# Optimization experiments

Hardware: AMD Instinct MI355X
Metric: run time of the kernel (lower is better)

Reference implementation:

```python
import jax, jax.numpy as jnp
import numpy as np
import math

H = 16          # num_attention_heads
DH = 64         # attention_head_size
HID = 1024      # hidden_size


def _rotate_half(x):
    # stack([-x[...,1::2], x[...,::2]], -1).reshape_as(x)
    return jnp.stack([-x[..., 1::2], x[..., ::2]], axis=-1).reshape(x.shape)


def _apply_rope(sinusoidal_pos, q, k):
    sin, cos = jnp.split(sinusoidal_pos, 2, axis=-1)            # [1,1,S,DH/2] each
    sin_pos = jnp.stack([sin, sin], axis=-1).reshape(sinusoidal_pos.shape)
    cos_pos = jnp.stack([cos, cos], axis=-1).reshape(sinusoidal_pos.shape)
    q = q * cos_pos + _rotate_half(q) * sin_pos
    k = k * cos_pos + _rotate_half(k) * sin_pos
    return q, k


def _split_heads(x):
    B, S, _ = x.shape
    return x.reshape(B, S, H, DH).transpose(0, 2, 1, 3)         # [B,H,S,DH]


def setup_inputs() -> dict:
    key = jax.random.key(0)
    ks = jax.random.split(key, 5)
    B, S = 4, 2048
    x = jax.random.normal(ks[0], (B, S, HID), dtype=jnp.float32)
    attention_mask = jnp.zeros((B, 1, 1, S), dtype=jnp.float32)
    sinusoidal_pos = jax.random.normal(ks[1], (1, 1, S, DH), dtype=jnp.float32)
    scale = 1.0 / math.sqrt(HID)
    Wq = jax.random.normal(ks[2], (HID, HID), dtype=jnp.float32) * scale
    Wk = jax.random.normal(ks[3], (HID, HID), dtype=jnp.float32) * scale
    Wv = jax.random.normal(ks[4], (HID, HID), dtype=jnp.float32) * scale
    bq = jnp.zeros((HID,), dtype=jnp.float32)
    bk = jnp.zeros((HID,), dtype=jnp.float32)
    bv = jnp.zeros((HID,), dtype=jnp.float32)
    return {"x": x, "attention_mask": attention_mask, "sinusoidal_pos": sinusoidal_pos,
            "Wq": Wq, "bq": bq, "Wk": Wk, "bk": bk, "Wv": Wv, "bv": bv}


def reference(x, attention_mask, sinusoidal_pos, Wq, bq, Wk, bk, Wv, bv):
    # QKV projections (torch Linear: x @ W.T + b)
    q = _split_heads(x @ Wq.T + bq)                             # [B,H,S,DH]
    k = _split_heads(x @ Wk.T + bk)
    v = _split_heads(x @ Wv.T + bv)
    q, k = _apply_rope(sinusoidal_pos, q, k)
    scores = jnp.einsum('bhsd,bhtd->bhst', q, k) / math.sqrt(DH) + attention_mask
    probs = jax.nn.softmax(scores, axis=-1)                     # dropout p=0.0 -> identity
    ctx = jnp.einsum('bhst,bhtd->bhsd', probs, v)               # [B,H,S,DH]
    B, _, S, _ = ctx.shape
    return ctx.transpose(0, 2, 1, 3).reshape(B, S, HID)
```

## Files before the change

### kernel.cpp

```cpp
#include <hip/hip_runtime.h>
#include <stdint.h>

#define BATCH 4
#define SEQ   2048
#define NHEAD 16
#define DHEAD 64
#define HID   1024

typedef __bf16 bf16x8 __attribute__((ext_vector_type(8)));
typedef __bf16 bf16x4 __attribute__((ext_vector_type(4)));
typedef float  f32x4  __attribute__((ext_vector_type(4)));
typedef short  s16x4  __attribute__((ext_vector_type(4)));

__device__ __forceinline__ bf16x8 load8f(const float* p) {
  const f32x4 a = ((const f32x4*)p)[0];
  const f32x4 b = ((const f32x4*)p)[1];
  bf16x8 r;
#pragma unroll
  for (int i = 0; i < 4; ++i) r[i] = (__bf16)a[i];
#pragma unroll
  for (int i = 0; i < 4; ++i) r[4 + i] = (__bf16)b[i];
  return r;
}

__device__ __forceinline__ s16x4 as_s16x4(bf16x4 v) {
  s16x4 r; __builtin_memcpy(&r, &v, 8); return r;
}

__device__ __forceinline__ void gload_lds16(const __bf16* g, __bf16* l) {
  __builtin_amdgcn_global_load_lds(
      (const __attribute__((address_space(1))) uint32_t*)g,
      (__attribute__((address_space(3))) uint32_t*)l,
      16, 0, 0);
}

#define XUNITS 1048576
#define WUNITS 131072

__global__ __launch_bounds__(256) void cvt_fused_kernel(
    const float* __restrict__ x,
    const float* __restrict__ Wq, const float* __restrict__ Wk,
    const float* __restrict__ Wv,
    __bf16* __restrict__ xb, __bf16* __restrict__ Wb) {
  const int i = blockIdx.x * 256 + threadIdx.x;
  const float* s;
  __bf16* d;
  if (i < XUNITS) {
    s = x + (size_t)i * 8;
    d = xb + (size_t)i * 8;
  } else {
    const int j = i - XUNITS;
    const int w = j >> 17;
    const int o = j & (WUNITS - 1);
    s = (w == 0 ? Wq : w == 1 ? Wk : Wv) + (size_t)o * 8;
    d = Wb + ((size_t)w << 20) + (size_t)o * 8;
  }
  *(bf16x8*)d = load8f(s);
}

#define ASTRIDE 40
#define BK 32

__global__ __launch_bounds__(512) void qkv_fused_kernel(
    const __bf16* __restrict__ xb, const __bf16* __restrict__ Wb,
    const float* __restrict__ bq, const float* __restrict__ bk,
    const float* __restrict__ bv, const float* __restrict__ sp,
    float* __restrict__ qout, __bf16* __restrict__ Kws, __bf16* __restrict__ Vws)
{
  const int d    = blockIdx.x + (blockIdx.y << 3);
  const int t    = (d & 7) * 64 + (d >> 3);
  const int n0   = (t & 7) * 128;
  const int m0   = (t >> 3) * 128;

  const int tid  = threadIdx.x;
  const int lane = tid & 63;
  const int quad = lane >> 4;
  const int l16  = lane & 15;
  const int wave = tid >> 6;
  const int wr   = wave >> 1, wc = wave & 1;

  __shared__ __align__(16) __bf16 As[2][128 * BK];
  __shared__ __align__(16) __bf16 Bs[3][2][128 * BK];

  const int srow = wave * 16 + (lane >> 2);
  const int scol = (lane & 3) * 8;
  const __bf16* aglb  = xb + (size_t)(m0 + srow) * HID + scol;
  const __bf16* bglb0 = Wb + (size_t)(n0 + srow) * HID + scol;
  const __bf16* bglb1 = bglb0 + (size_t)HID * HID;
  const __bf16* bglb2 = bglb0 + (size_t)2 * HID * HID;
  const int woff = wave * 512;

  f32x4 aQ[2][4], aK[2][4], aV[2][4];
  const f32x4 z = {0.f, 0.f, 0.f, 0.f};
#pragma unroll
  for (int i = 0; i < 2; ++i)
#pragma unroll
    for (int j = 0; j < 4; ++j) { aQ[i][j] = z; aK[i][j] = z; aV[i][j] = z; }

  gload_lds16(aglb,  &As[0][woff]);
  gload_lds16(bglb0, &Bs[0][0][woff]);
  gload_lds16(bglb1, &Bs[1][0][woff]);
  gload_lds16(bglb2, &Bs[2][0][woff]);
  __syncthreads();

#pragma unroll 1
  for (int k0 = 0; k0 < HID; k0 += 2 * BK) {
    {
      gload_lds16(aglb  + (k0 + BK), &As[1][woff]);
      gload_lds16(bglb0 + (k0 + BK), &Bs[0][1][woff]);
      gload_lds16(bglb1 + (k0 + BK), &Bs[1][1][woff]);
      gload_lds16(bglb2 + (k0 + BK), &Bs[2][1][woff]);

      bf16x8 af[2];
#pragma unroll
      for (int mt = 0; mt < 2; ++mt)
        af[mt] = *(const bf16x8*)(&As[0][(wr * 32 + mt * 16 + l16) * BK + quad * 8]);
      {
        bf16x8 bfr[4];
#pragma unroll
        for (int nt = 0; nt < 4; ++nt)
          bfr[nt] = *(const bf16x8*)(&Bs[0][0][(wc * 64 + nt * 16 + l16) * BK + quad * 8]);
#pragma unroll
        for (int mt = 0; mt < 2; ++mt)
#pragma unroll
          for (int nt = 0; nt < 4; ++nt)
            aQ[mt][nt] = __builtin_amdgcn_mfma_f32_16x16x32_bf16(af[mt], bfr[nt], aQ[mt][nt], 0, 0, 0);
      }
      {
        bf16x8 bfr[4];
#pragma unroll
        for (int nt = 0; nt < 4; ++nt)
          bfr[nt] = *(const bf16x8*)(&Bs[1][0][(wc * 64 + nt * 16 + l16) * BK + quad * 8]);
#pragma unroll
        for (int mt = 0; mt < 2; ++mt)
#pragma unroll
          for (int nt = 0; nt < 4; ++nt)
            aK[mt][nt] = __builtin_amdgcn_mfma_f32_16x16x32_bf16(af[mt], bfr[nt], aK[mt][nt], 0, 0, 0);
      }
      {
        bf16x8 bfr[4];
#pragma unroll
        for (int nt = 0; nt < 4; ++nt)
          bfr[nt] = *(const bf16x8*)(&Bs[2][0][(wc * 64 + nt * 16 + l16) * BK + quad * 8]);
#pragma unroll
        for (int mt = 0; mt < 2; ++mt)
#pragma unroll
          for (int nt = 0; nt < 4; ++nt)
            aV[mt][nt] = __builtin_amdgcn_mfma_f32_16x16x32_bf16(bfr[nt], af[mt], aV[mt][nt], 0, 0, 0);
      }
      __syncthreads();
    }
    {
      if (k0 + 2 * BK < HID) {
        gload_lds16(aglb  + (k0 + 2 * BK), &As[0][woff]);
        gload_lds16(bglb0 + (k0 + 2 * BK), &Bs[0][0][woff]);
        gload_lds16(bglb1 + (k0 + 2 * BK), &Bs[1][0][woff]);
        gload_lds16(bglb2 + (k0 + 2 * BK), &Bs[2][0][woff]);
      }

      bf16x8 af[2];
#pragma unroll
      for (int mt = 0; mt < 2; ++mt)
        af[mt] = *(const bf16x8*)(&As[1][(wr * 32 + mt * 16 + l16) * BK + quad * 8]);
      {
        bf16x8 bfr[4];
#pragma unroll
        for (int nt = 0; nt < 4; ++nt)
          bfr[nt] = *(const bf16x8*)(&Bs[0][1][(wc * 64 + nt * 16 + l16) * BK + quad * 8]);
#pragma unroll
        for (int mt = 0; mt < 2; ++mt)
#pragma unroll
          for (int nt = 0; nt < 4; ++nt)
            aQ[mt][nt] = __builtin_amdgcn_mfma_f32_16x16x32_bf16(af[mt], bfr[nt], aQ[mt][nt], 0, 0, 0);
      }
      {
        bf16x8 bfr[4];
#pragma unroll
        for (int nt = 0; nt < 4; ++nt)
          bfr[nt] = *(const bf16x8*)(&Bs[1][1][(wc * 64 + nt * 16 + l16) * BK + quad * 8]);
#pragma unroll
        for (int mt = 0; mt < 2; ++mt)
#pragma unroll
          for (int nt = 0; nt < 4; ++nt)
            aK[mt][nt] = __builtin_amdgcn_mfma_f32_16x16x32_bf16(af[mt], bfr[nt], aK[mt][nt], 0, 0, 0);
      }
      {
        bf16x8 bfr[4];
#pragma unroll
        for (int nt = 0; nt < 4; ++nt)
          bfr[nt] = *(const bf16x8*)(&Bs[2][1][(wc * 64 + nt * 16 + l16) * BK + quad * 8]);
#pragma unroll
        for (int mt = 0; mt < 2; ++mt)
#pragma unroll
          for (int nt = 0; nt < 4; ++nt)
            aV[mt][nt] = __builtin_amdgcn_mfma_f32_16x16x32_bf16(bfr[nt], af[mt], aV[mt][nt], 0, 0, 0);
      }
      __syncthreads();
    }
  }

#pragma unroll
  for (int mt = 0; mt < 2; ++mt) {
#pragma unroll
    for (int nt = 0; nt < 4; ++nt) {
      const int n = n0 + wc * 64 + nt * 16 + l16;
      const int h = n >> 6, dd = n & 63;
      const float bval = bq[n];
#pragma unroll
      for (int v = 0; v < 4; ++v) {
        const int m = m0 + wr * 32 + mt * 16 + quad * 4 + v;
        const int b = m >> 11, s = m & (SEQ - 1);
        float val = aQ[mt][nt][v] + bval;
        float p  = __shfl_xor(val, 1);
        float sn = sp[s * 64 + (dd >> 1)];
        float cs = sp[s * 64 + 32 + (dd >> 1)];
        val = val * cs + ((dd & 1) ? p : -p) * sn;
        qout[((size_t)b * SEQ + s) * HID + n] = val;
      }
    }
  }
#pragma unroll
  for (int mt = 0; mt < 2; ++mt) {
#pragma unroll
    for (int nt = 0; nt < 4; ++nt) {
      const int n = n0 + wc * 64 + nt * 16 + l16;
      const int h = n >> 6, dd = n & 63;
      const float bval = bk[n];
#pragma unroll
      for (int v = 0; v < 4; ++v) {
        const int m = m0 + wr * 32 + mt * 16 + quad * 4 + v;
        const int b = m >> 11, s = m & (SEQ - 1);
        float val = aK[mt][nt][v] + bval;
        float p  = __shfl_xor(val, 1);
        float sn = sp[s * 64 + (dd >> 1)];
        float cs = sp[s * 64 + 32 + (dd >> 1)];
        val = val * cs + ((dd & 1) ? p : -p) * sn;
        Kws[(((size_t)b * NHEAD + h) * SEQ + s) * DHEAD + dd] = (__bf16)val;
      }
    }
  }
#pragma unroll
  for (int mt = 0; mt < 2; ++mt) {
#pragma unroll
    for (int nt = 0; nt < 4; ++nt) {
      const int m = m0 + wr * 32 + mt * 16 + l16;
      const int b = m >> 11, s = m & (SEQ - 1);
#pragma unroll
      for (int v = 0; v < 4; ++v) {
        const int n = n0 + wc * 64 + nt * 16 + quad * 4 + v;
        const int h = n >> 6, dd = n & 63;
        float val = aV[mt][nt][v] + bv[n];
        Vws[(((size_t)b * NHEAD + h) * DHEAD + dd) * SEQ + s] = (__bf16)val;
      }
    }
  }
}

__global__ __launch_bounds__(512) void qkv_f32_kernel(
    const float* __restrict__ x,
    const float* __restrict__ Wq, const float* __restrict__ bq,
    const float* __restrict__ Wk, const float* __restrict__ bk,
    const float* __restrict__ Wv, const float* __restrict__ bv,
    const float* __restrict__ sp,
    float* __restrict__ qout, __bf16* __restrict__ Kws, __bf16* __restrict__ Vws)
{
  const int widx = blockIdx.z;
  const float* __restrict__ W    = (widx == 0) ? Wq : (widx == 1) ? Wk : Wv;
  const float* __restrict__ bias = (widx == 0) ? bq : (widx == 1) ? bk : bv;

  const int m0   = blockIdx.y * 128;
  const int n0   = blockIdx.x * 128;
  const int tid  = threadIdx.x;
  const int lane = tid & 63;
  const int quad = lane >> 4;
  const int l16  = lane & 15;
  const int wave = tid >> 6;
  const int wr   = wave >> 1, wc = wave & 1;

  __shared__ __align__(16) __bf16 As[128 * ASTRIDE];
  __shared__ __align__(16) __bf16 Bs[128 * ASTRIDE];

  const int srow = tid >> 2;
  const int scb  = tid & 3;

  f32x4 acc[2][4];
  const f32x4 z = {0.f, 0.f, 0.f, 0.f};
#pragma unroll
  for (int i = 0; i < 2; ++i)
#pragma unroll
    for (int j = 0; j < 4; ++j) acc[i][j] = z;

  bf16x8 areg = load8f(x + (size_t)(m0 + srow) * HID + scb * 8);
  bf16x8 breg = load8f(W + (size_t)(n0 + srow) * HID + scb * 8);

  for (int k0 = 0; k0 < HID; k0 += 32) {
    __syncthreads();
    *(bf16x8*)(As + srow * ASTRIDE + scb * 8) = areg;
    *(bf16x8*)(Bs + srow * ASTRIDE + scb * 8) = breg;
    __syncthreads();

    if (k0 + 32 < HID) {
      areg = load8f(x + (size_t)(m0 + srow) * HID + (k0 + 32) + scb * 8);
      breg = load8f(W + (size_t)(n0 + srow) * HID + (k0 + 32) + scb * 8);
    }

    bf16x8 af[2], bfr[4];
#pragma unroll
    for (int mt = 0; mt < 2; ++mt)
      af[mt] = *(const bf16x8*)(As + (wr * 32 + mt * 16 + l16) * ASTRIDE + quad * 8);
#pragma unroll
    for (int nt = 0; nt < 4; ++nt)
      bfr[nt] = *(const bf16x8*)(Bs + (wc * 64 + nt * 16 + l16) * ASTRIDE + quad * 8);

    if (widx < 2) {
#pragma unroll
      for (int mt = 0; mt < 2; ++mt)
#pragma unroll
        for (int nt = 0; nt < 4; ++nt)
          acc[mt][nt] = __builtin_amdgcn_mfma_f32_16x16x32_bf16(af[mt], bfr[nt], acc[mt][nt], 0, 0, 0);
    } else {
#pragma unroll
      for (int mt = 0; mt < 2; ++mt)
#pragma unroll
        for (int nt = 0; nt < 4; ++nt)
          acc[mt][nt] = __builtin_amdgcn_mfma_f32_16x16x32_bf16(bfr[nt], af[mt], acc[mt][nt], 0, 0, 0);
    }
  }

  if (widx < 2) {
#pragma unroll
    for (int mt = 0; mt < 2; ++mt) {
#pragma unroll
      for (int nt = 0; nt < 4; ++nt) {
        const int n = n0 + wc * 64 + nt * 16 + l16;
        const int h = n >> 6, dd = n & 63;
        const float bval = bias[n];
#pragma unroll
        for (int v = 0; v < 4; ++v) {
          const int m = m0 + wr * 32 + mt * 16 + quad * 4 + v;
          const int b = m >> 11, s = m & (SEQ - 1);
          float val = acc[mt][nt][v] + bval;
          float p  = __shfl_xor(val, 1);
          float sn = sp[s * 64 + (dd >> 1)];
          float cs = sp[s * 64 + 32 + (dd >> 1)];
          val = val * cs + ((dd & 1) ? p : -p) * sn;
          if (widx == 0) {
            qout[((size_t)b * SEQ + s) * HID + n] = val;
          } else {
            Kws[(((size_t)b * NHEAD + h) * SEQ + s) * DHEAD + dd] = (__bf16)val;
          }
        }
      }
    }
  } else {
#pragma unroll
    for (int mt = 0; mt < 2; ++mt) {
#pragma unroll
      for (int nt = 0; nt < 4; ++nt) {
        const int m = m0 + wr * 32 + mt * 16 + l16;
        const int b = m >> 11, s = m & (SEQ - 1);
#pragma unroll
        for (int v = 0; v < 4; ++v) {
          const int n = n0 + wc * 64 + nt * 16 + quad * 4 + v;
          const int h = n >> 6, dd = n & 63;
          float val = acc[mt][nt][v] + bias[n];
          Vws[(((size_t)b * NHEAD + h) * DHEAD + dd) * SEQ + s] = (__bf16)val;
        }
      }
    }
  }
}

#define KT 64
#define QSTR 72
#define LOG2E 1.44269504088896340736f
#define PSHIFT 12.0f

__global__ __launch_bounds__(512) void attn_kernel(
    float* __restrict__ qo,
    const __bf16* __restrict__ Kws, const __bf16* __restrict__ Vws,
    const float* __restrict__ mask)
{
  const int dsw  = blockIdx.x + (blockIdx.y << 4);
  const int tsw  = (dsw & 7) * 128 + (dsw >> 3);
  const int bh   = tsw >> 4;
  const int q0   = (tsw & 15) * 128;

  const int b    = bh >> 4, h = bh & 15;
  const int tid  = threadIdx.x;
  const int lane = tid & 63;
  const int wave = tid >> 6;
  const int quad = lane >> 4;
  const int l16  = lane & 15;

  __shared__ __align__(16) __bf16 Ks[64 * QSTR];
  __shared__ __align__(16) __bf16 Vts[64 * QSTR];

  const __bf16* kbase = Kws + (size_t)bh * SEQ * DHEAD;
  const __bf16* vbase = Vws + (size_t)bh * DHEAD * SEQ;

  bf16x8 qf[2];
#pragma unroll
  for (int ks = 0; ks < 2; ++ks)
    qf[ks] = load8f(qo + ((size_t)b * SEQ + q0 + wave * 16 + l16) * HID
                       + h * DHEAD + ks * 32 + quad * 8);

  f32x4 o_acc[4];
  const f32x4 z = {0.f, 0.f, 0.f, 0.f};
#pragma unroll
  for (int i = 0; i < 4; ++i) o_acc[i] = z;
  float l_part = 0.f;

  const int qrow = tid >> 3;
  const int qcb  = tid & 7;

  bf16x8 kreg = *(const bf16x8*)(kbase + (size_t)qrow * DHEAD + qcb * 8);
  bf16x8 vreg = *(const bf16x8*)(vbase + (size_t)qrow * SEQ + qcb * 8);

  const float SC2 = 0.125f * LOG2E;

  for (int t0 = 0; t0 < SEQ; t0 += KT) {
    *(bf16x8*)(Ks  + qrow * QSTR + qcb * 8) = kreg;
    *(bf16x8*)(Vts + qrow * QSTR + qcb * 8) = vreg;
    __syncthreads();

    if (t0 + KT < SEQ) {
      kreg = *(const bf16x8*)(kbase + (size_t)(t0 + KT + qrow) * DHEAD + qcb * 8);
      vreg = *(const bf16x8*)(vbase + (size_t)qrow * SEQ + (t0 + KT) + qcb * 8);
    }

    f32x4 sc[4];
#pragma unroll
    for (int nt = 0; nt < 4; ++nt) sc[nt] = z;

    __builtin_amdgcn_s_setprio(1);
#pragma unroll
    for (int ks = 0; ks < 2; ++ks) {
      bf16x8 kf[4];
#pragma unroll
      for (int nt = 0; nt < 4; ++nt)
        kf[nt] = *(const bf16x8*)(Ks + (nt * 16 + l16) * QSTR + ks * 32 + quad * 8);
#pragma unroll
      for (int nt = 0; nt < 4; ++nt)
        sc[nt] = __builtin_amdgcn_mfma_f32_16x16x32_bf16(kf[nt], qf[ks], sc[nt], 0, 0, 0);
    }
    __builtin_amdgcn_s_setprio(0);

    f32x4 mv4[4];
#pragma unroll
    for (int nt = 0; nt < 4; ++nt)
      mv4[nt] = *(const f32x4*)(mask + b * SEQ + t0 + nt * 16 + quad * 4);

    s16x4 pf[4];
#pragma unroll
    for (int nt = 0; nt < 4; ++nt) {
      bf16x4 pk;
#pragma unroll
      for (int v = 0; v < 4; ++v) {
        const float p = __builtin_amdgcn_exp2f(sc[nt][v] * SC2 + mv4[nt][v] * LOG2E - PSHIFT);
        l_part += p;
        pk[v] = (__bf16)p;
      }
      pf[nt] = as_s16x4(pk);
    }

    __builtin_amdgcn_s_setprio(1);
#pragma unroll
    for (int nt = 0; nt < 4; ++nt) {
      bf16x4 vf4[4];
#pragma unroll
      for (int db = 0; db < 4; ++db)
        vf4[db] = *(const bf16x4*)(Vts + (db * 16 + l16) * QSTR + nt * 16 + quad * 4);
#pragma unroll
      for (int db = 0; db < 4; ++db)
        o_acc[db] = __builtin_amdgcn_mfma_f32_16x16x16bf16_1k(
            as_s16x4(vf4[db]), pf[nt], o_acc[db], 0, 0, 0);
    }
    __builtin_amdgcn_s_setprio(0);
    __syncthreads();
  }

  l_part += __shfl_xor(l_part, 16);
  l_part += __shfl_xor(l_part, 32);
  const float inv = 1.0f / l_part;

  const int s = q0 + wave * 16 + l16;
  float* op = qo + ((size_t)b * SEQ + s) * HID + h * DHEAD + quad * 4;
#pragma unroll
  for (int db = 0; db < 4; ++db) {
    f32x4 val = o_acc[db];
    val[0] *= inv; val[1] *= inv; val[2] *= inv; val[3] *= inv;
    *(f32x4*)(op + db * 16) = val;
  }
}

extern "C" void kernel_launch(void* const* d_in, const int* in_sizes, int n_in,
                              void* d_out, int out_size, void* d_ws, size_t ws_size,
                              hipStream_t stream) {
  const float* x    = (const float*)d_in[0];
  const float* mask = (const float*)d_in[1];
  const float* sp   = (const float*)d_in[2];
  const float* Wq   = (const float*)d_in[3];
  const float* bq   = (const float*)d_in[4];
  const float* Wk   = (const float*)d_in[5];
  const float* bk   = (const float*)d_in[6];
  const float* Wv   = (const float*)d_in[7];
  const float* bv   = (const float*)d_in[8];
  float* out = (float*)d_out;

  const size_t per = (size_t)BATCH * NHEAD * SEQ * DHEAD;
  const size_t wel = (size_t)3 * HID * HID;
  __bf16* Kws = (__bf16*)d_ws;
  __bf16* Vws = Kws + per;

  const size_t need = (2 * per + per + wel) * sizeof(__bf16);
  if (ws_size >= need) {
    __bf16* xb = Vws + per;
    __bf16* Wb = xb + per;
    cvt_fused_kernel<<<5632, 256, 0, stream>>>(x, Wq, Wk, Wv, xb, Wb);
    qkv_fused_kernel<<<dim3(8, 64), 512, 0, stream>>>(
        xb, Wb, bq, bk, bv, sp, out, Kws, Vws);
  } else {
    qkv_f32_kernel<<<dim3(8, 64, 3), 512, 0, stream>>>(
        x, Wq, bq, Wk, bk, Wv, bv, sp, out, Kws, Vws);
  }
  attn_kernel<<<dim3(16, 64), 512, 0, stream>>>(out, Kws, Vws, mask);
}
```

Before: 303.1 us.

## Double query rows per wave in attention to reuse K/V tiles

Each attention block now covers 256 query rows instead of 128: every wave handles two 16-row query subtiles and reuses the same K and V fragments from shared memory for both. This halves the grid and the total K/V global and LDS traffic per query, and gives the MFMA units more independent work per wave. In exchange it raises register use (doubled accumulators and score tiles), which may lower occupancy, and the smaller grid of 512 blocks may fill the GPU less evenly.

Result: slower. 319.3 us (+5.3%).

```diff
diff --git a/kernel.cpp b/kernel.cpp
--- a/kernel.cpp
+++ b/kernel.cpp
@@ -381,10 +381,10 @@
     const __bf16* __restrict__ Kws, const __bf16* __restrict__ Vws,
     const float* __restrict__ mask)
 {
-  const int dsw  = blockIdx.x + (blockIdx.y << 4);
-  const int tsw  = (dsw & 7) * 128 + (dsw >> 3);
-  const int bh   = tsw >> 4;
-  const int q0   = (tsw & 15) * 128;
+  const int dsw  = blockIdx.x + (blockIdx.y << 3);
+  const int tsw  = (dsw & 7) * 64 + (dsw >> 3);
+  const int bh   = tsw >> 3;
+  const int q0   = (tsw & 7) * 256;
 
   const int b    = bh >> 4, h = bh & 15;
   const int tid  = threadIdx.x;
@@ -399,17 +399,21 @@
   const __bf16* kbase = Kws + (size_t)bh * SEQ * DHEAD;
   const __bf16* vbase = Vws + (size_t)bh * DHEAD * SEQ;
 
-  bf16x8 qf[2];
-#pragma unroll
-  for (int ks = 0; ks < 2; ++ks)
-    qf[ks] = load8f(qo + ((size_t)b * SEQ + q0 + wave * 16 + l16) * HID
-                       + h * DHEAD + ks * 32 + quad * 8);
-
-  f32x4 o_acc[4];
+  bf16x8 qf[2][2];
+#pragma unroll
+  for (int mq = 0; mq < 2; ++mq)
+#pragma unroll
+    for (int ks = 0; ks < 2; ++ks)
+      qf[mq][ks] = load8f(qo + ((size_t)b * SEQ + q0 + wave * 32 + mq * 16 + l16) * HID
+                             + h * DHEAD + ks * 32 + quad * 8);
+
+  f32x4 o_acc[2][4];
   const f32x4 z = {0.f, 0.f, 0.f, 0.f};
 #pragma unroll
-  for (int i = 0; i < 4; ++i) o_acc[i] = z;
-  float l_part = 0.f;
+  for (int mq = 0; mq < 2; ++mq)
+#pragma unroll
+    for (int i = 0; i < 4; ++i) o_acc[mq][i] = z;
+  float l_part[2] = {0.f, 0.f};
 
   const int qrow = tid >> 3;
   const int qcb  = tid & 7;
@@ -429,9 +433,11 @@
       vreg = *(const bf16x8*)(vbase + (size_t)qrow * SEQ + (t0 + KT) + qcb * 8);
     }
 
-    f32x4 sc[4];
-#pragma unroll
-    for (int nt = 0; nt < 4; ++nt) sc[nt] = z;
+    f32x4 sc[2][4];
+#pragma unroll
+    for (int mq = 0; mq < 2; ++mq)
+#pragma unroll
+      for (int nt = 0; nt < 4; ++nt) sc[mq][nt] = z;
 
     __builtin_amdgcn_s_setprio(1);
 #pragma unroll
@@ -441,8 +447,10 @@
       for (int nt = 0; nt < 4; ++nt)
         kf[nt] = *(const bf16x8*)(Ks + (nt * 16 + l16) * QSTR + ks * 32 + quad * 8);
 #pragma unroll
-      for (int nt = 0; nt < 4; ++nt)
-        sc[nt] = __builtin_amdgcn_mfma_f32_16x16x32_bf16(kf[nt], qf[ks], sc[nt], 0, 0, 0);
+      for (int mq = 0; mq < 2; ++mq)
+#pragma unroll
+        for (int nt = 0; nt < 4; ++nt)
+          sc[mq][nt] = __builtin_amdgcn_mfma_f32_16x16x32_bf16(kf[nt], qf[mq][ks], sc[mq][nt], 0, 0, 0);
     }
     __builtin_amdgcn_s_setprio(0);
 
@@ -451,17 +459,20 @@
     for (int nt = 0; nt < 4; ++nt)
       mv4[nt] = *(const f32x4*)(mask + b * SEQ + t0 + nt * 16 + quad * 4);
 
-    s16x4 pf[4];
-#pragma unroll
-    for (int nt = 0; nt < 4; ++nt) {
-      bf16x4 pk;
-#pragma unroll
-      for (int v = 0; v < 4; ++v) {
-        const float p = __builtin_amdgcn_exp2f(sc[nt][v] * SC2 + mv4[nt][v] * LOG2E - PSHIFT);
-        l_part += p;
-        pk[v] = (__bf16)p;
-      }
-      pf[nt] = as_s16x4(pk);
+    s16x4 pf[2][4];
+#pragma unroll
+    for (int mq = 0; mq < 2; ++mq) {
+#pragma unroll
+      for (int nt = 0; nt < 4; ++nt) {
+        bf16x4 pk;
+#pragma unroll
+        for (int v = 0; v < 4; ++v) {
+          const float p = __builtin_amdgcn_exp2f(sc[mq][nt][v] * SC2 + mv4[nt][v] * LOG2E - PSHIFT);
+          l_part[mq] += p;
+          pk[v] = (__bf16)p;
+        }
+        pf[mq][nt] = as_s16x4(pk);
+      }
     }
 
     __builtin_amdgcn_s_setprio(1);
@@ -472,25 +483,30 @@
       for (int db = 0; db < 4; ++db)
         vf4[db] = *(const bf16x4*)(Vts + (db * 16 + l16) * QSTR + nt * 16 + quad * 4);
 #pragma unroll
-      for (int db = 0; db < 4; ++db)
-        o_acc[db] = __builtin_amdgcn_mfma_f32_16x16x16bf16_1k(
-            as_s16x4(vf4[db]), pf[nt], o_acc[db], 0, 0, 0);
+      for (int mq = 0; mq < 2; ++mq)
+#pragma unroll
+        for (int db = 0; db < 4; ++db)
+          o_acc[mq][db] = __builtin_amdgcn_mfma_f32_16x16x16bf16_1k(
+              as_s16x4(vf4[db]), pf[mq][nt], o_acc[mq][db], 0, 0, 0);
     }
     __builtin_amdgcn_s_setprio(0);
     __syncthreads();
   }
 
-  l_part += __shfl_xor(l_part, 16);
-  l_part += __shfl_xor(l_part, 32);
-  const float inv = 1.0f / l_part;
-
-  const int s = q0 + wave * 16 + l16;
-  float* op = qo + ((size_t)b * SEQ + s) * HID + h * DHEAD + quad * 4;
-#pragma unroll
-  for (int db = 0; db < 4; ++db) {
-    f32x4 val = o_acc[db];
-    val[0] *= inv; val[1] *= inv; val[2] *= inv; val[3] *= inv;
-    *(f32x4*)(op + db * 16) = val;
+#pragma unroll
+  for (int mq = 0; mq < 2; ++mq) {
+    float l = l_part[mq];
+    l += __shfl_xor(l, 16);
+    l += __shfl_xor(l, 32);
+    const float inv = 1.0f / l;
+    const int s = q0 + wave * 32 + mq * 16 + l16;
+    float* op = qo + ((size_t)b * SEQ + s) * HID + h * DHEAD + quad * 4;
+#pragma unroll
+    for (int db = 0; db < 4; ++db) {
+      f32x4 val = o_acc[mq][db];
+      val[0] *= inv; val[1] *= inv; val[2] *= inv; val[3] *= inv;
+      *(f32x4*)(op + db * 16) = val;
+    }
   }
 }
 
@@ -524,5 +540,5 @@
     qkv_f32_kernel<<<dim3(8, 64, 3), 512, 0, stream>>>(
         x, Wq, bq, Wk, bk, Wv, bv, sp, out, Kws, Vws);
   }
-  attn_kernel<<<dim3(16, 64), 512, 0, stream>>>(out, Kws, Vws, mask);
-}
+  attn_kernel<<<dim3(8, 64), 512, 0, stream>>>(out, Kws, Vws, mask);
+}
```
